# Kernel tuning notes

Hardware: AMD Instinct MI355X
Metric: run time of the kernel (lower is better)

## Reference

```python
import jax, jax.numpy as jnp
import numpy as np

N, S, W, H = 256, 64, 256, 32   # node_num, sensor_num, slide_win, gru_hid_size
ALPHA = 0.2
NEG = -9e15


def gat(h, adj, Wm, a):
    """pyGAT GraphAttentionLayer (concat=False, dropout=0 / eval).
    h: [..., M, din], adj: [..., M, M], Wm: [..., din, dout], a: [..., 2*dout]."""
    Wh = jnp.einsum('...mi,...io->...mo', h, Wm)
    dout = Wm.shape[-1]
    f1 = jnp.einsum('...mo,...o->...m', Wh, a[..., :dout])
    f2 = jnp.einsum('...mo,...o->...m', Wh, a[..., dout:])
    e = jax.nn.leaky_relu(f1[..., :, None] + f2[..., None, :], negative_slope=ALPHA)
    att = jax.nn.softmax(jnp.where(adj > 0, e, NEG), axis=-1)
    return jnp.einsum('...mk,...ko->...mo', att, Wh)


def gru_cell(h, x, Wih, Whh, bih, bhh):
    # per-node batched torch GRU cell; gate order r, z, n
    gi = jnp.einsum('ngi,ni->ng', Wih, x) + bih
    gh = jnp.einsum('ngh,nh->ng', Whh, h) + bhh
    ir, iz, inn = jnp.split(gi, 3, axis=-1)
    hr, hz, hn = jnp.split(gh, 3, axis=-1)
    r = jax.nn.sigmoid(ir + hr)
    z = jax.nn.sigmoid(iz + hz)
    n = jnp.tanh(inn + r * hn)
    return (1.0 - z) * n + z * h


def gru2(xseq, h0, Wih0, Whh0, bih0, bhh0, Wih1, Whh1, bih1, bhh1):
    # xseq: [N, S, Din] (seq axis = sensor axis), h0: [2, N, H] -> ([N,S,H], [2,N,H])
    def step(carry, x_t):
        h0c, h1c = carry
        h0n = gru_cell(h0c, x_t, Wih0, Whh0, bih0, bhh0)
        h1n = gru_cell(h1c, h0n, Wih1, Whh1, bih1, bhh1)
        return (h0n, h1n), h1n
    (h0f, h1f), ys = jax.lax.scan(step, (h0[0], h0[1]), jnp.swapaxes(xseq, 0, 1))
    return jnp.swapaxes(ys, 0, 1), jnp.stack([h0f, h1f])


def setup_inputs():
    key = jax.random.key(0)
    ks = jax.random.split(key, 32)
    def rn(k, shape, scale=0.05):
        return jax.random.normal(k, shape, dtype=jnp.float32) * scale
    inp = {}
    inp['x'] = jax.random.normal(ks[0], (N, S, W), dtype=jnp.float32)
    inp['Feature_adj_sub'] = jax.random.randint(ks[1], (N, S, S), 0, 2).astype(jnp.float32)
    inp['Time_adj_sub'] = jax.random.randint(ks[2], (N, W, W), 0, 2).astype(jnp.float32)
    inp['adj'] = jax.random.randint(ks[3], (N, N), 0, 2).astype(jnp.float32)
    inp['H_pre'] = jax.random.normal(ks[4], (2, N, H), dtype=jnp.float32)
    # per-node GAT params (stacked over nodes)
    inp['Fatt_W'] = rn(ks[5], (N, W, W)); inp['Fatt_a'] = rn(ks[6], (N, 2 * W))
    inp['Tatt_W'] = rn(ks[7], (N, S, S)); inp['Tatt_a'] = rn(ks[8], (N, 2 * S))
    # per-node 2-layer GRU params
    inp['Wih0'] = rn(ks[9], (N, 3 * H, 3 * W)); inp['Whh0'] = rn(ks[10], (N, 3 * H, H))
    inp['bih0'] = rn(ks[11], (N, 3 * H)); inp['bhh0'] = rn(ks[12], (N, 3 * H))
    inp['Wih1'] = rn(ks[13], (N, 3 * H, H)); inp['Whh1'] = rn(ks[14], (N, 3 * H, H))
    inp['bih1'] = rn(ks[15], (N, 3 * H)); inp['bhh1'] = rn(ks[16], (N, 3 * H))
    # per-node 3-layer FC
    inp['fc1_w'] = rn(ks[17], (N, H, H)); inp['fc1_b'] = rn(ks[18], (N, H))
    inp['fc2_w'] = rn(ks[19], (N, H, H)); inp['fc2_b'] = rn(ks[20], (N, H))
    inp['fc3_w'] = rn(ks[21], (N, 1, H)); inp['fc3_b'] = rn(ks[22], (N, 1))
    # global output GATs
    inp['oW'] = rn(ks[23], (S, S)); inp['oa'] = rn(ks[24], (2 * S,))
    inp['o1W'] = rn(ks[25], (S, S)); inp['o1a'] = rn(ks[26], (2 * S,))
    inp['o2W'] = rn(ks[27], (2 * S, S)); inp['o2a'] = rn(ks[28], (2 * S,))
    return inp


def reference(x, Feature_adj_sub, Time_adj_sub, adj, H_pre,
              Fatt_W, Fatt_a, Tatt_W, Tatt_a,
              Wih0, Whh0, bih0, bhh0, Wih1, Whh1, bih1, bhh1,
              fc1_w, fc1_b, fc2_w, fc2_b, fc3_w, fc3_b,
              oW, oa, o1W, o1a, o2W, o2a):
    # batched over all nodes at once (replaces Python loop over node_num)
    Fat = gat(x, Feature_adj_sub, Fatt_W, Fatt_a)                    # [N,S,W]
    Tat = gat(jnp.swapaxes(x, 1, 2), Time_adj_sub, Tatt_W, Tatt_a)   # [N,W,S]
    cat_at = jnp.concatenate([Fat, jnp.swapaxes(Tat, 1, 2), x], axis=-1)  # [N,S,3W]
    gru_out, cat_H = gru2(cat_at, H_pre, Wih0, Whh0, bih0, bhh0,
                          Wih1, Whh1, bih1, bhh1)                    # [N,S,H],[2,N,H]
    h = jax.nn.relu(jnp.einsum('nsh,nkh->nsk', gru_out, fc1_w) + fc1_b[:, None, :])
    h = jax.nn.relu(jnp.einsum('nsh,nkh->nsk', h, fc2_w) + fc2_b[:, None, :])
    ct = (jnp.einsum('nsh,nkh->nsk', h, fc3_w) + fc3_b[:, None, :])[..., 0]  # [N,S]
    out = gat(ct, adj, oW, oa)
    out1 = gat(ct, adj, o1W, o1a)
    finalout = gat(jnp.concatenate([out, out1], axis=-1), adj, o2W, o2a)
    return finalout, cat_H
```

## Files before the change

kernel.cpp:

```cpp
#include <hip/hip_runtime.h>
#include <hip/hip_bf16.h>

__device__ __forceinline__ float sigf(float x){ return __builtin_amdgcn_rcpf(1.f+__expf(-x)); }
__device__ __forceinline__ float tanhfa(float x){
  return 1.f - 2.f*__builtin_amdgcn_rcpf(1.f + __expf(2.f*x));
}

#define ALPHA 0.2f
#define NEGV  -9e15f


__device__ __forceinline__ void gl2lds16(const float* g, float* l){
  __builtin_amdgcn_global_load_lds(
      (const __attribute__((address_space(1))) void*)g,
      (__attribute__((address_space(3))) void*)l, 16, 0, 0);
}

__global__ __launch_bounds__(256) void k_mask(const float* __restrict__ src,
                                              unsigned* __restrict__ dst, int nelem){
  const int stride = gridDim.x * blockDim.x;
  const int lane = threadIdx.x & 63;
  for (int e = blockIdx.x*blockDim.x + threadIdx.x; e < nelem; e += stride){
    unsigned long long m = __ballot(src[e] > 0.f);
    if (lane == 0)       dst[e >> 5] = (unsigned)m;
    else if (lane == 32) dst[e >> 5] = (unsigned)(m >> 32);
  }
}

__global__ __launch_bounds__(256) void k3_wht(const float* __restrict__ x,
                                              const float* __restrict__ TW,
                                              const float* __restrict__ Ta,
                                              float* __restrict__ WhTt,
                                              float* __restrict__ Tf1p,
                                              float* __restrict__ Tf2p){
  const int n = blockIdx.x >> 1, ch = blockIdx.x & 1, c0 = ch*32;
  const int tid = threadIdx.x;
  __shared__ float Wm[64][36];
  __shared__ float as1[32], as2[32];
  for (int idx = tid; idx < 2048; idx += 256){
    int k = idx >> 5, cc = idx & 31;
    Wm[k][cc] = TW[n*4096 + k*64 + c0 + cc];
  }
  if (tid < 32){ as1[tid] = Ta[n*128 + c0 + tid]; as2[tid] = Ta[n*128 + 64 + c0 + tid]; }
  __syncthreads();
  const int i = tid;
  const float* xn = x + n*16384;
  float acc[32];
#pragma unroll
  for (int c = 0; c < 32; ++c) acc[c] = 0.f;
#pragma unroll 2
  for (int k = 0; k < 64; ++k){
    float xv = xn[k*256 + i];
    const float* wr = &Wm[k][0];
#pragma unroll
    for (int c = 0; c < 32; ++c) acc[c] = fmaf(xv, wr[c], acc[c]);
  }
  float f1 = 0.f, f2 = 0.f;
#pragma unroll
  for (int c = 0; c < 32; ++c){ f1 = fmaf(acc[c], as1[c], f1); f2 = fmaf(acc[c], as2[c], f2); }
  Tf1p[ch*65536 + n*256 + i] = f1;
  Tf2p[ch*65536 + n*256 + i] = f2;
  float* o = WhTt + n*16384;
#pragma unroll
  for (int c = 0; c < 32; ++c) o[(c0+c)*256 + i] = acc[c];
}

__global__ __launch_bounds__(256) void k4_tat(const float* __restrict__ WhTt,
                                              const float* __restrict__ Tf1p,
                                              const float* __restrict__ Tf2p,
                                              const unsigned* __restrict__ maskT,
                                              float* __restrict__ TatT){
  const int n = blockIdx.x >> 1, ch = blockIdx.x & 1, c0 = ch*32;
  const int i = threadIdx.x;
  __shared__ float wt[8192];
  __shared__ float f2s[256];
  __shared__ float wmax[4];
  {
    const int w = i >> 6, l = i & 63;
    const float* src = WhTt + n*16384 + c0*256 + w*2048 + l*4;
    float* dst = &wt[w*2048];
#pragma unroll
    for (int r = 0; r < 8; ++r) gl2lds16(src + r*256, dst + r*256);
  }
  const float f1  = Tf1p[n*256 + i] + Tf1p[65536 + n*256 + i];
  const float f2v = Tf2p[n*256 + i] + Tf2p[65536 + n*256 + i];
  f2s[i] = f2v;
  unsigned mw[8];
#pragma unroll
  for (int w = 0; w < 8; ++w) mw[w] = maskT[n*2048 + i*8 + w];
  float wm = f2v;
#pragma unroll
  for (int d = 1; d < 64; d <<= 1) wm = fmaxf(wm, __shfl_xor(wm, d));
  if ((i & 63) == 0) wmax[i >> 6] = wm;
  asm volatile("s_waitcnt vmcnt(0)" ::: "memory");
  __syncthreads();
  const float mb = fmaxf(fmaxf(wmax[0], wmax[1]), fmaxf(wmax[2], wmax[3]));
  const float tm = f1 + mb;
  const float m  = (tm > 0.f) ? tm : ALPHA*tm;
  float acc[32];
#pragma unroll
  for (int c = 0; c < 32; ++c) acc[c] = 0.f;
  float s = 0.f;
#pragma unroll 2
  for (int jb = 0; jb < 64; ++jb){
    const float4 f2q = *(const float4*)&f2s[jb*4];
    const unsigned mk = mw[jb >> 3];
    const int sh = (jb & 7) * 4;
    float t0 = f1 + f2q.x; t0 = (t0 > 0.f) ? t0 : ALPHA*t0;
    float t1 = f1 + f2q.y; t1 = (t1 > 0.f) ? t1 : ALPHA*t1;
    float t2 = f1 + f2q.z; t2 = (t2 > 0.f) ? t2 : ALPHA*t2;
    float t3 = f1 + f2q.w; t3 = (t3 > 0.f) ? t3 : ALPHA*t3;
    const float e0 = ((mk >> (sh+0)) & 1u) ? __expf(t0 - m) : 0.f;
    const float e1 = ((mk >> (sh+1)) & 1u) ? __expf(t1 - m) : 0.f;
    const float e2 = ((mk >> (sh+2)) & 1u) ? __expf(t2 - m) : 0.f;
    const float e3 = ((mk >> (sh+3)) & 1u) ? __expf(t3 - m) : 0.f;
    s += (e0 + e1) + (e2 + e3);
#pragma unroll
    for (int c = 0; c < 32; ++c){
      const float4 wv = *(const float4*)&wt[c*256 + jb*4];
      acc[c] = fmaf(e0, wv.x, fmaf(e1, wv.y, fmaf(e2, wv.z, fmaf(e3, wv.w, acc[c]))));
    }
  }
  const float inv = (s > 0.f) ? __builtin_amdgcn_rcpf(s) : 0.f;
  float* o = TatT + n*16384;
#pragma unroll
  for (int c = 0; c < 32; ++c) o[(c0+c)*256 + i] = acc[c] * inv;
}

__global__ __launch_bounds__(256) void k1_whf(const float* __restrict__ x,
                                              const float* __restrict__ FW,
                                              float* __restrict__ WhF){
  const int n = blockIdx.x >> 1, ch = blockIdx.x & 1, c0 = ch*128;
  const int tid = threadIdx.x;
  __shared__ float xt[16384];
  {
    const int w = tid >> 6, l = tid & 63;
    const float* xg = x + n*16384 + w*4096 + l*4;
    float* ld = &xt[w*4096];
#pragma unroll
    for (int j = 0; j < 16; ++j) gl2lds16(xg + j*256, ld + j*256);
  }
  asm volatile("s_waitcnt vmcnt(0)" ::: "memory");
  __syncthreads();
  const int cq = tid & 31, iq = tid >> 5;
  const int cc = c0 + cq*4;
  const float* Wn = FW + (size_t)n*65536 + cc;
  const float* xrow = &xt[iq*8*256];
  float acc[8][4];
#pragma unroll
  for (int i = 0; i < 8; ++i)
#pragma unroll
    for (int c = 0; c < 4; ++c) acc[i][c] = 0.f;
#pragma unroll 2
  for (int k4 = 0; k4 < 64; ++k4){
    const float4 w0 = *(const float4*)&Wn[(4*k4+0)*256];
    const float4 w1 = *(const float4*)&Wn[(4*k4+1)*256];
    const float4 w2 = *(const float4*)&Wn[(4*k4+2)*256];
    const float4 w3 = *(const float4*)&Wn[(4*k4+3)*256];
#pragma unroll
    for (int i = 0; i < 8; ++i){
      const float4 xv = *(const float4*)&xrow[i*256 + 4*k4];
      acc[i][0] = fmaf(xv.x, w0.x, acc[i][0]); acc[i][0] = fmaf(xv.y, w1.x, acc[i][0]);
      acc[i][0] = fmaf(xv.z, w2.x, acc[i][0]); acc[i][0] = fmaf(xv.w, w3.x, acc[i][0]);
      acc[i][1] = fmaf(xv.x, w0.y, acc[i][1]); acc[i][1] = fmaf(xv.y, w1.y, acc[i][1]);
      acc[i][1] = fmaf(xv.z, w2.y, acc[i][1]); acc[i][1] = fmaf(xv.w, w3.y, acc[i][1]);
      acc[i][2] = fmaf(xv.x, w0.z, acc[i][2]); acc[i][2] = fmaf(xv.y, w1.z, acc[i][2]);
      acc[i][2] = fmaf(xv.z, w2.z, acc[i][2]); acc[i][2] = fmaf(xv.w, w3.z, acc[i][2]);
      acc[i][3] = fmaf(xv.x, w0.w, acc[i][3]); acc[i][3] = fmaf(xv.y, w1.w, acc[i][3]);
      acc[i][3] = fmaf(xv.z, w2.w, acc[i][3]); acc[i][3] = fmaf(xv.w, w3.w, acc[i][3]);
    }
  }
  float* o = WhF + n*16384 + cc;
#pragma unroll
  for (int i = 0; i < 8; ++i)
    *(float4*)&o[(iq*8 + i)*256] = make_float4(acc[i][0], acc[i][1], acc[i][2], acc[i][3]);
}

__global__ __launch_bounds__(512) void k2_fat(const float* __restrict__ WhF,
                                              const float* __restrict__ Fa,
                                              const float* __restrict__ Fadj,
                                              float* __restrict__ Fat){
  const int n = blockIdx.x, tid = threadIdx.x;
  __shared__ float attT[64][68];
  __shared__ float f1s[64], f2s[64];
  __shared__ float part[64][8][2];
  const float* Wh = WhF + n*16384;
  {
    int i = tid >> 3, q = tid & 7;
    const float* an = Fa + n*512;
    float p1 = 0.f, p2 = 0.f;
    for (int cc = 0; cc < 32; ++cc){
      int c2 = q*32 + cc;
      float w = Wh[i*256 + c2];
      p1 = fmaf(w, an[c2], p1);
      p2 = fmaf(w, an[256 + c2], p2);
    }
    part[i][q][0] = p1; part[i][q][1] = p2;
  }
  __syncthreads();
  if (tid < 64){
    float s1 = 0.f, s2 = 0.f;
#pragma unroll
    for (int q = 0; q < 8; ++q){ s1 += part[tid][q][0]; s2 += part[tid][q][1]; }
    f1s[tid] = s1; f2s[tid] = s2;
  }
  __syncthreads();
  if (tid < 64){
    const int r = tid;
    const float f1 = f1s[r];
    const float* adjr = Fadj + n*4096 + r*64;
    unsigned m0 = 0, m1 = 0;
#pragma unroll
    for (int j = 0; j < 32; ++j) if (adjr[j] > 0.f) m0 |= (1u << j);
#pragma unroll
    for (int j = 0; j < 32; ++j) if (adjr[32+j] > 0.f) m1 |= (1u << j);
    float m = -INFINITY;
#pragma unroll
    for (int j = 0; j < 64; ++j){
      float e = f1 + f2s[j]; e = (e > 0.f) ? e : ALPHA*e;
      unsigned bit = (j < 32) ? ((m0 >> j) & 1u) : ((m1 >> (j-32)) & 1u);
      e = bit ? e : NEGV;
      m = fmaxf(m, e);
    }
    float s = 0.f;
#pragma unroll
    for (int j = 0; j < 64; ++j){
      float e = f1 + f2s[j]; e = (e > 0.f) ? e : ALPHA*e;
      unsigned bit = (j < 32) ? ((m0 >> j) & 1u) : ((m1 >> (j-32)) & 1u);
      e = bit ? e : NEGV;
      s += __expf(e - m);
    }
    const float inv = 1.f / s;
#pragma unroll
    for (int j = 0; j < 64; ++j){
      float e = f1 + f2s[j]; e = (e > 0.f) ? e : ALPHA*e;
      unsigned bit = (j < 32) ? ((m0 >> j) & 1u) : ((m1 >> (j-32)) & 1u);
      e = bit ? e : NEGV;
      attT[j][r] = __expf(e - m) * inv;
    }
  }
  __syncthreads();
  const int c = tid & 255, ih = tid >> 8;
  float acc[32];
#pragma unroll
  for (int i = 0; i < 32; ++i) acc[i] = 0.f;
#pragma unroll 2
  for (int j = 0; j < 64; ++j){
    float w = Wh[j*256 + c];
    const float* ar = &attT[j][ih*32];
#pragma unroll
    for (int i = 0; i < 32; ++i) acc[i] = fmaf(ar[i], w, acc[i]);
  }
  float* o = Fat + n*16384;
#pragma unroll
  for (int i = 0; i < 32; ++i) o[(ih*32 + i)*256 + c] = acc[i];
}

__global__ __launch_bounds__(256) void k5_gi0(const float* __restrict__ Fat,
                                              const float* __restrict__ TatT,
                                              const float* __restrict__ x,
                                              const float* __restrict__ Wih0,
                                              float* __restrict__ P0,
                                              float* __restrict__ P1,
                                              float* __restrict__ P2){
  const int n = blockIdx.x & 255, s = blockIdx.x >> 8;
  const int tid = threadIdx.x;
  const int l = tid & 63, w = tid >> 6;
  const int a = tid & 31, b = tid >> 5;
  __shared__ float cl[2][2048];
  __shared__ float wl[2][3072];
  const float* src = (s == 0) ? (Fat + n*16384)
                   : (s == 1) ? (TatT + n*16384)
                              : (x + n*16384);
  const float* Wseg = Wih0 + (size_t)n*73728 + s*256;
  const int lr = l >> 3, lc = l & 7, sc = lc ^ lr;
  const float* cg0 = src + (16*w + lr)*256 + sc*4;
  const float* cg1 = cg0 + 8*256;
  const float* wg0 = Wseg + (size_t)(24*w + lr)*768 + lc*4;
  const float* wg1 = wg0 + (size_t)8*768;
  const float* wg2 = wg0 + (size_t)16*768;

#define K5_STAGE(BF, K0) do {                       \
    gl2lds16(cg0 + (K0), &cl[BF][512*w]);           \
    gl2lds16(cg1 + (K0), &cl[BF][512*w + 256]);     \
    gl2lds16(wg0 + (K0), &wl[BF][768*w]);           \
    gl2lds16(wg1 + (K0), &wl[BF][768*w + 256]);     \
    gl2lds16(wg2 + (K0), &wl[BF][768*w + 512]);     \
  } while (0)

  float acc[12][2];
#pragma unroll
  for (int gi = 0; gi < 12; ++gi){ acc[gi][0] = 0.f; acc[gi][1] = 0.f; }

  int bf = 0;
  K5_STAGE(0, 0);
  const int ax4 = (a & 7) << 2;
#pragma unroll 1
  for (int kt = 0; kt < 8; ++kt){
    if (kt < 7){
      K5_STAGE(bf ^ 1, (kt + 1) * 32);
      asm volatile("s_waitcnt vmcnt(5)" ::: "memory");
    } else {
      asm volatile("s_waitcnt vmcnt(0)" ::: "memory");
    }
    __builtin_amdgcn_s_barrier();
    const float* clb  = &cl[bf][a*32];
    const float* clb2 = &cl[bf][(a+32)*32];
    const float* wlb  = &wl[bf][b*384];
#pragma unroll
    for (int k4 = 0; k4 < 8; ++k4){
      const int j4 = (k4 << 2) ^ ax4;
      const float4 c0 = *(const float4*)&clb[j4];
      const float4 c1 = *(const float4*)&clb2[j4];
#pragma unroll
      for (int gi = 0; gi < 12; ++gi){
        const float4 wv = *(const float4*)&wlb[gi*32 + (k4 << 2)];
        float a0 = acc[gi][0], a1 = acc[gi][1];
        a0 = fmaf(wv.x, c0.x, a0); a1 = fmaf(wv.x, c1.x, a1);
        a0 = fmaf(wv.y, c0.y, a0); a1 = fmaf(wv.y, c1.y, a1);
        a0 = fmaf(wv.z, c0.z, a0); a1 = fmaf(wv.z, c1.z, a1);
        a0 = fmaf(wv.w, c0.w, a0); a1 = fmaf(wv.w, c1.w, a1);
        acc[gi][0] = a0; acc[gi][1] = a1;
      }
    }
    __builtin_amdgcn_s_barrier();
    bf ^= 1;
  }
#undef K5_STAGE
  float* o = (s == 0) ? (P0 + n*16384)
           : (s == 1) ? (P1 + n*16384)
                      : (P2 + n*8192);
#pragma unroll
  for (int q = 0; q < 3; ++q){
    *(float4*)&o[a*96 + b*12 + q*4] =
        make_float4(acc[4*q][0], acc[4*q+1][0], acc[4*q+2][0], acc[4*q+3][0]);
    *(float4*)&o[(a+32)*96 + b*12 + q*4] =
        make_float4(acc[4*q][1], acc[4*q+1][1], acc[4*q+2][1], acc[4*q+3][1]);
  }
}

__global__ __launch_bounds__(128) void k6_gru(const float* __restrict__ G0,
                                              const float* __restrict__ G1,
                                              const float* __restrict__ G2,
                                              const float* __restrict__ Hpre,
                                              const float* __restrict__ Whh0,
                                              const float* __restrict__ bih0,
                                              const float* __restrict__ bhh0,
                                              const float* __restrict__ Wih1,
                                              const float* __restrict__ Whh1,
                                              const float* __restrict__ bih1,
                                              const float* __restrict__ bhh1,
                                              const float* __restrict__ fc1w,
                                              const float* __restrict__ fc1b,
                                              const float* __restrict__ fc2w,
                                              const float* __restrict__ fc2b,
                                              const float* __restrict__ fc3w,
                                              const float* __restrict__ fc3b,
                                              float* __restrict__ ct,
                                              float* __restrict__ dout){
  const int n = blockIdx.x, tid = threadIdx.x;
  const int wid = tid >> 6, l = tid & 63;
  const int g2 = l & 31, co = (l >> 5) * 16;
  __shared__ float ginS[6144];
  __shared__ float h0buf[2][32];
  __shared__ float h1buf[2][32];
  __shared__ float hist[64][33];
  __shared__ float Wst[32][33];
  __shared__ float b1s[32], b2s[32], w3s[32];
  {
    const float4* p0 = (const float4*)(G0 + n*16384);
    const float4* p1 = (const float4*)(G1 + n*16384);
    const float4* p2 = (const float4*)(G2 + n*8192);
    float4* gs = (float4*)ginS;
#pragma unroll
    for (int j = 0; j < 12; ++j){
      int idx = j*128 + tid;
      float4 a = p0[idx], b = p1[idx], c = p2[idx];
      gs[idx] = make_float4(a.x+b.x+c.x, a.y+b.y+c.y, a.z+b.z+c.z, a.w+b.w+c.w);
    }
  }
  if (tid < 32){
    b1s[tid] = fc1b[n*32 + tid];
    b2s[tid] = fc2b[n*32 + tid];
    w3s[tid] = fc3w[n*32 + tid];
  }
  for (int idx = tid; idx < 1024; idx += 128) Wst[idx>>5][idx&31] = fc1w[n*1024 + idx];
  float wr_[16], wz_[16], wn_[16];
  float ur_[16], uz_[16], un_[16];
  {
    const float* WA = (wid == 0) ? (Whh0 + n*3072) : (Wih1 + n*3072);
#pragma unroll
    for (int q = 0; q < 4; ++q){
      float4 v;
      v = *(const float4*)(WA + g2*32 + co + 4*q);       wr_[4*q]=v.x; wr_[4*q+1]=v.y; wr_[4*q+2]=v.z; wr_[4*q+3]=v.w;
      v = *(const float4*)(WA + (32+g2)*32 + co + 4*q);  wz_[4*q]=v.x; wz_[4*q+1]=v.y; wz_[4*q+2]=v.z; wz_[4*q+3]=v.w;
      v = *(const float4*)(WA + (64+g2)*32 + co + 4*q);  wn_[4*q]=v.x; wn_[4*q+1]=v.y; wn_[4*q+2]=v.z; wn_[4*q+3]=v.w;
    }
    if (wid == 1){
      const float* WB = Whh1 + n*3072;
#pragma unroll
      for (int q = 0; q < 4; ++q){
        float4 v;
        v = *(const float4*)(WB + g2*32 + co + 4*q);       ur_[4*q]=v.x; ur_[4*q+1]=v.y; ur_[4*q+2]=v.z; ur_[4*q+3]=v.w;
        v = *(const float4*)(WB + (32+g2)*32 + co + 4*q);  uz_[4*q]=v.x; uz_[4*q+1]=v.y; uz_[4*q+2]=v.z; uz_[4*q+3]=v.w;
        v = *(const float4*)(WB + (64+g2)*32 + co + 4*q);  un_[4*q]=v.x; un_[4*q+1]=v.y; un_[4*q+2]=v.z; un_[4*q+3]=v.w;
      }
    }
  }
  const float* bip = (wid == 0) ? bih0 : bih1;
  const float* bhp = (wid == 0) ? bhh0 : bhh1;
  const float br = bip[n*96 + g2], bz = bip[n*96 + 32 + g2], bn = bip[n*96 + 64 + g2];
  const float cr = bhp[n*96 + g2], cz = bhp[n*96 + 32 + g2], cn = bhp[n*96 + 64 + g2];
  const float* hp = (wid == 0) ? (Hpre + n*32) : (Hpre + 8192 + n*32);
  float hown = hp[g2];
  float hs[16];
#pragma unroll
  for (int q = 0; q < 4; ++q){
    float4 v = *(const float4*)&hp[co + 4*q];
    hs[4*q]=v.x; hs[4*q+1]=v.y; hs[4*q+2]=v.z; hs[4*q+3]=v.w;
  }
  for (int s = 0; s < 65; ++s){
    __syncthreads();
    if (wid == 0){
      if (s < 64){
        const float gr = ginS[s*96 + g2], gz = ginS[s*96 + 32 + g2], gn = ginS[s*96 + 64 + g2];
        if (s > 0){
#pragma unroll
          for (int q = 0; q < 4; ++q){
            float4 v = *(const float4*)&h0buf[(s-1)&1][co + 4*q];
            hs[4*q]=v.x; hs[4*q+1]=v.y; hs[4*q+2]=v.z; hs[4*q+3]=v.w;
          }
        }
        float pr = 0.f, pz = 0.f, pn = 0.f;
#pragma unroll
        for (int j = 0; j < 16; ++j){
          pr = fmaf(wr_[j], hs[j], pr);
          pz = fmaf(wz_[j], hs[j], pz);
          pn = fmaf(wn_[j], hs[j], pn);
        }
        pr += __shfl_xor(pr, 32);
        pz += __shfl_xor(pz, 32);
        pn += __shfl_xor(pn, 32);
        const float r = sigf(gr + br + pr + cr);
        const float z = sigf(gz + bz + pz + cz);
        const float nn = tanhfa(gn + bn + r*(pn + cn));
        hown = (1.f - z)*nn + z*hown;
        if (l < 32) h0buf[s & 1][g2] = hown;
      }
    } else {
      if (s >= 1){
        const int t = s - 1;
        if (s > 1){
#pragma unroll
          for (int q = 0; q < 4; ++q){
            float4 v = *(const float4*)&h1buf[(s-1)&1][co + 4*q];
            hs[4*q]=v.x; hs[4*q+1]=v.y; hs[4*q+2]=v.z; hs[4*q+3]=v.w;
          }
        }
        float hx[16];
#pragma unroll
        for (int q = 0; q < 4; ++q){
          float4 v = *(const float4*)&h0buf[(s-1)&1][co + 4*q];
          hx[4*q]=v.x; hx[4*q+1]=v.y; hx[4*q+2]=v.z; hx[4*q+3]=v.w;
        }
        float qr = 0.f, qz = 0.f, qn = 0.f, sr = 0.f, sz = 0.f, sn = 0.f;
#pragma unroll
        for (int j = 0; j < 16; ++j){
          qr = fmaf(wr_[j], hx[j], qr);  sr = fmaf(ur_[j], hs[j], sr);
          qz = fmaf(wz_[j], hx[j], qz);  sz = fmaf(uz_[j], hs[j], sz);
          qn = fmaf(wn_[j], hx[j], qn);  sn = fmaf(un_[j], hs[j], sn);
        }
        float vr = qr + sr; vr += __shfl_xor(vr, 32);
        float vz = qz + sz; vz += __shfl_xor(vz, 32);
        qn += __shfl_xor(qn, 32);
        sn += __shfl_xor(sn, 32);
        const float r1 = sigf(vr + br + cr);
        const float z1 = sigf(vz + bz + cz);
        const float n1 = tanhfa(qn + bn + r1*(sn + cn));
        hown = (1.f - z1)*n1 + z1*hown;
        if (l < 32){ h1buf[s & 1][g2] = hown; hist[t][g2] = hown; }
      }
    }
  }
  if (wid == 0 && l < 32) dout[16384 + n*32 + g2] = hown;
  if (wid == 1 && l < 32) dout[16384 + 8192 + n*32 + g2] = hown;
  __syncthreads();
  float r1a[32];
  if (tid < 64){
    float hr[32];
#pragma unroll
    for (int k = 0; k < 32; ++k) hr[k] = hist[tid][k];
#pragma unroll
    for (int k = 0; k < 32; ++k){
      float a0=0.f,a1=0.f,a2=0.f,a3=0.f;
#pragma unroll
      for (int q = 0; q < 32; q += 4){
        a0 = fmaf(hr[q],   Wst[k][q],   a0);
        a1 = fmaf(hr[q+1], Wst[k][q+1], a1);
        a2 = fmaf(hr[q+2], Wst[k][q+2], a2);
        a3 = fmaf(hr[q+3], Wst[k][q+3], a3);
      }
      float v = b1s[k] + ((a0+a1)+(a2+a3));
      r1a[k] = v > 0.f ? v : 0.f;
    }
  }
  __syncthreads();
  for (int idx = tid; idx < 1024; idx += 128) Wst[idx>>5][idx&31] = fc2w[n*1024 + idx];
  __syncthreads();
  if (tid < 64){
    float r2a[32];
#pragma unroll
    for (int k = 0; k < 32; ++k){
      float a0=0.f,a1=0.f,a2=0.f,a3=0.f;
#pragma unroll
      for (int q = 0; q < 32; q += 4){
        a0 = fmaf(r1a[q],   Wst[k][q],   a0);
        a1 = fmaf(r1a[q+1], Wst[k][q+1], a1);
        a2 = fmaf(r1a[q+2], Wst[k][q+2], a2);
        a3 = fmaf(r1a[q+3], Wst[k][q+3], a3);
      }
      float v = b2s[k] + ((a0+a1)+(a2+a3));
      r2a[k] = v > 0.f ? v : 0.f;
    }
    float v = fc3b[n];
#pragma unroll
    for (int k = 0; k < 32; ++k) v = fmaf(r2a[k], w3s[k], v);
    ct[n*64 + tid] = v;
  }
}

__global__ __launch_bounds__(256) void k8a(const float* __restrict__ ct,
                                           const float* __restrict__ W0,
                                           const float* __restrict__ a0,
                                           const float* __restrict__ W1,
                                           const float* __restrict__ a1,
                                           float* __restrict__ WhABt,
                                           float* __restrict__ OF1,
                                           float* __restrict__ OF2){
  const int gat = blockIdx.x >> 2, rq = blockIdx.x & 3, r0 = rq*64;
  const int tid = threadIdx.x;
  const int ii = tid & 63, cq = tid >> 6;
  __shared__ float ctl[64][65];
  __shared__ float Wl[64][68];
  __shared__ float a1s[64], a2s[64];
  __shared__ float red[64][4][2];
  const float* W = gat ? W1 : W0;
  const float* aa = gat ? a1 : a0;
  for (int idx = tid; idx < 4096; idx += 256){
    int i2 = idx >> 6, k = idx & 63;
    ctl[i2][k] = ct[(r0 + i2)*64 + k];
  }
  for (int idx = tid; idx < 4096; idx += 256){
    int k = idx >> 6, c = idx & 63;
    Wl[k][c] = W[k*64 + c];
  }
  if (tid < 64){ a1s[tid] = aa[tid]; a2s[tid] = aa[64 + tid]; }
  __syncthreads();
  float acc[16];
#pragma unroll
  for (int c = 0; c < 16; ++c) acc[c] = 0.f;
#pragma unroll 2
  for (int k = 0; k < 64; ++k){
    float v = ctl[ii][k];
    const float* wr = &Wl[k][cq*16];
#pragma unroll
    for (int c = 0; c < 16; ++c) acc[c] = fmaf(v, wr[c], acc[c]);
  }
  float p1 = 0.f, p2 = 0.f;
#pragma unroll
  for (int c = 0; c < 16; ++c){
    p1 = fmaf(acc[c], a1s[cq*16 + c], p1);
    p2 = fmaf(acc[c], a2s[cq*16 + c], p2);
  }
  red[ii][cq][0] = p1; red[ii][cq][1] = p2;
  float* o = WhABt + gat*16384;
#pragma unroll
  for (int c = 0; c < 16; ++c) o[(cq*16 + c)*256 + r0 + ii] = acc[c];
  __syncthreads();
  if (cq == 0){
    OF1[gat*256 + r0 + ii] = red[ii][0][0] + red[ii][1][0] + red[ii][2][0] + red[ii][3][0];
    OF2[gat*256 + r0 + ii] = red[ii][0][1] + red[ii][1][1] + red[ii][2][1] + red[ii][3][1];
  }
}

__global__ __launch_bounds__(256) void k8b(const float* __restrict__ WhABt,
                                           const float* __restrict__ OF1,
                                           const float* __restrict__ OF2,
                                           const unsigned* __restrict__ maskA,
                                           float* __restrict__ OUTT){
  const int gat = blockIdx.x >> 2, c0 = (blockIdx.x & 3) * 16;
  const int i = threadIdx.x;
  __shared__ float wt[4096];
  __shared__ float f2s[256];
  __shared__ float wmax[4];
  {
    const int w = i >> 6, l = i & 63;
    const float* src = WhABt + gat*16384 + c0*256 + w*1024 + l*4;
    float* dst = &wt[w*1024];
#pragma unroll
    for (int r = 0; r < 4; ++r) gl2lds16(src + r*256, dst + r*256);
  }
  const float f1  = OF1[gat*256 + i];
  const float f2v = OF2[gat*256 + i];
  f2s[i] = f2v;
  unsigned mw[8];
#pragma unroll
  for (int w = 0; w < 8; ++w) mw[w] = maskA[i*8 + w];
  float wm = f2v;
#pragma unroll
  for (int d = 1; d < 64; d <<= 1) wm = fmaxf(wm, __shfl_xor(wm, d));
  if ((i & 63) == 0) wmax[i >> 6] = wm;
  asm volatile("s_waitcnt vmcnt(0)" ::: "memory");
  __syncthreads();
  const float mb = fmaxf(fmaxf(wmax[0], wmax[1]), fmaxf(wmax[2], wmax[3]));
  const float tm = f1 + mb;
  const float m  = (tm > 0.f) ? tm : ALPHA*tm;
  float acc[16];
#pragma unroll
  for (int c = 0; c < 16; ++c) acc[c] = 0.f;
  float s = 0.f;
#pragma unroll 2
  for (int jb = 0; jb < 64; ++jb){
    const float4 f2q = *(const float4*)&f2s[jb*4];
    const unsigned mk = mw[jb >> 3];
    const int sh = (jb & 7) * 4;
    float t0 = f1 + f2q.x; t0 = (t0 > 0.f) ? t0 : ALPHA*t0;
    float t1 = f1 + f2q.y; t1 = (t1 > 0.f) ? t1 : ALPHA*t1;
    float t2 = f1 + f2q.z; t2 = (t2 > 0.f) ? t2 : ALPHA*t2;
    float t3 = f1 + f2q.w; t3 = (t3 > 0.f) ? t3 : ALPHA*t3;
    const float e0 = ((mk >> (sh+0)) & 1u) ? __expf(t0 - m) : 0.f;
    const float e1 = ((mk >> (sh+1)) & 1u) ? __expf(t1 - m) : 0.f;
    const float e2 = ((mk >> (sh+2)) & 1u) ? __expf(t2 - m) : 0.f;
    const float e3 = ((mk >> (sh+3)) & 1u) ? __expf(t3 - m) : 0.f;
    s += (e0 + e1) + (e2 + e3);
#pragma unroll
    for (int c = 0; c < 16; ++c){
      const float4 wv = *(const float4*)&wt[c*256 + jb*4];
      acc[c] = fmaf(e0, wv.x, fmaf(e1, wv.y, fmaf(e2, wv.z, fmaf(e3, wv.w, acc[c]))));
    }
  }
  const float inv = (s > 0.f) ? __builtin_amdgcn_rcpf(s) : 0.f;
#pragma unroll
  for (int c = 0; c < 16; ++c) OUTT[gat*16384 + (c0+c)*256 + i] = acc[c] * inv;
}

__global__ __launch_bounds__(256) void k8c(const float* __restrict__ OUTT,
                                           const float* __restrict__ W2,
                                           const float* __restrict__ a2,
                                           float* __restrict__ Wh2,
                                           float* __restrict__ F1B,
                                           float* __restrict__ F2B){
  const int r0 = blockIdx.x * 32;
  const int tid = threadIdx.x;
  const int ii = tid & 31, cq = tid >> 5;
  __shared__ float W2l[128][68];
  __shared__ float a1s[64], a2s[64];
  __shared__ float red[32][8][2];
  for (int idx = tid; idx < 8192; idx += 256){
    int k = idx >> 6, c = idx & 63;
    W2l[k][c] = W2[k*64 + c];
  }
  if (tid < 64){ a1s[tid] = a2[tid]; a2s[tid] = a2[64 + tid]; }
  __syncthreads();
  float acc[8];
#pragma unroll
  for (int c = 0; c < 8; ++c) acc[c] = 0.f;
#pragma unroll 2
  for (int k = 0; k < 128; ++k){
    float v = OUTT[(k >> 6)*16384 + (k & 63)*256 + r0 + ii];
    const float* wr = &W2l[k][cq*8];
#pragma unroll
    for (int c = 0; c < 8; ++c) acc[c] = fmaf(v, wr[c], acc[c]);
  }
  float p1 = 0.f, p2 = 0.f;
#pragma unroll
  for (int c = 0; c < 8; ++c){
    p1 = fmaf(acc[c], a1s[cq*8 + c], p1);
    p2 = fmaf(acc[c], a2s[cq*8 + c], p2);
  }
  red[ii][cq][0] = p1; red[ii][cq][1] = p2;
#pragma unroll
  for (int c = 0; c < 8; ++c) Wh2[(cq*8 + c)*256 + r0 + ii] = acc[c];
  __syncthreads();
  if (cq == 0){
    float s1 = 0.f, s2 = 0.f;
#pragma unroll
    for (int q = 0; q < 8; ++q){ s1 += red[ii][q][0]; s2 += red[ii][q][1]; }
    F1B[r0 + ii] = s1; F2B[r0 + ii] = s2;
  }
}

__global__ __launch_bounds__(256) void k8d(const float* __restrict__ Wh2,
                                           const float* __restrict__ F1B,
                                           const float* __restrict__ F2B,
                                           const unsigned* __restrict__ maskA,
                                           float* __restrict__ dOut){
  const int c0 = blockIdx.x * 16;
  const int i = threadIdx.x;
  __shared__ float wt[4096];
  __shared__ float f2s[256];
  __shared__ float wmax[4];
  {
    const int w = i >> 6, l = i & 63;
    const float* src = Wh2 + c0*256 + w*1024 + l*4;
    float* dst = &wt[w*1024];
#pragma unroll
    for (int r = 0; r < 4; ++r) gl2lds16(src + r*256, dst + r*256);
  }
  const float f1  = F1B[i];
  const float f2v = F2B[i];
  f2s[i] = f2v;
  unsigned mw[8];
#pragma unroll
  for (int w = 0; w < 8; ++w) mw[w] = maskA[i*8 + w];
  float wm = f2v;
#pragma unroll
  for (int d = 1; d < 64; d <<= 1) wm = fmaxf(wm, __shfl_xor(wm, d));
  if ((i & 63) == 0) wmax[i >> 6] = wm;
  asm volatile("s_waitcnt vmcnt(0)" ::: "memory");
  __syncthreads();
  const float mb = fmaxf(fmaxf(wmax[0], wmax[1]), fmaxf(wmax[2], wmax[3]));
  const float tm = f1 + mb;
  const float m  = (tm > 0.f) ? tm : ALPHA*tm;
  float acc[16];
#pragma unroll
  for (int c = 0; c < 16; ++c) acc[c] = 0.f;
  float s = 0.f;
#pragma unroll 2
  for (int jb = 0; jb < 64; ++jb){
    const float4 f2q = *(const float4*)&f2s[jb*4];
    const unsigned mk = mw[jb >> 3];
    const int sh = (jb & 7) * 4;
    float t0 = f1 + f2q.x; t0 = (t0 > 0.f) ? t0 : ALPHA*t0;
    float t1 = f1 + f2q.y; t1 = (t1 > 0.f) ? t1 : ALPHA*t1;
    float t2 = f1 + f2q.z; t2 = (t2 > 0.f) ? t2 : ALPHA*t2;
    float t3 = f1 + f2q.w; t3 = (t3 > 0.f) ? t3 : ALPHA*t3;
    const float e0 = ((mk >> (sh+0)) & 1u) ? __expf(t0 - m) : 0.f;
    const float e1 = ((mk >> (sh+1)) & 1u) ? __expf(t1 - m) : 0.f;
    const float e2 = ((mk >> (sh+2)) & 1u) ? __expf(t2 - m) : 0.f;
    const float e3 = ((mk >> (sh+3)) & 1u) ? __expf(t3 - m) : 0.f;
    s += (e0 + e1) + (e2 + e3);
#pragma unroll
    for (int c = 0; c < 16; ++c){
      const float4 wv = *(const float4*)&wt[c*256 + jb*4];
      acc[c] = fmaf(e0, wv.x, fmaf(e1, wv.y, fmaf(e2, wv.z, fmaf(e3, wv.w, acc[c]))));
    }
  }
  const float inv = (s > 0.f) ? __builtin_amdgcn_rcpf(s) : 0.f;
#pragma unroll
  for (int c = 0; c < 16; ++c) dOut[i*64 + c0 + c] = acc[c] * inv;
}

extern "C" void kernel_launch(void* const* d_in, const int* in_sizes, int n_in,
                              void* d_out, int out_size, void* d_ws, size_t ws_size,
                              hipStream_t stream){
  (void)in_sizes; (void)n_in; (void)out_size; (void)ws_size;
  const float* x     = (const float*)d_in[0];
  const float* Fadj  = (const float*)d_in[1];
  const float* Tadj  = (const float*)d_in[2];
  const float* adj   = (const float*)d_in[3];
  const float* Hpre  = (const float*)d_in[4];
  const float* FattW = (const float*)d_in[5];
  const float* Fatta = (const float*)d_in[6];
  const float* TattW = (const float*)d_in[7];
  const float* Tatta = (const float*)d_in[8];
  const float* Wih0  = (const float*)d_in[9];
  const float* Whh0  = (const float*)d_in[10];
  const float* bih0  = (const float*)d_in[11];
  const float* bhh0  = (const float*)d_in[12];
  const float* Wih1  = (const float*)d_in[13];
  const float* Whh1  = (const float*)d_in[14];
  const float* bih1  = (const float*)d_in[15];
  const float* bhh1  = (const float*)d_in[16];
  const float* fc1w  = (const float*)d_in[17];
  const float* fc1b  = (const float*)d_in[18];
  const float* fc2w  = (const float*)d_in[19];
  const float* fc2b  = (const float*)d_in[20];
  const float* fc3w  = (const float*)d_in[21];
  const float* fc3b  = (const float*)d_in[22];
  const float* oW    = (const float*)d_in[23];
  const float* oa    = (const float*)d_in[24];
  const float* o1W   = (const float*)d_in[25];
  const float* o1a   = (const float*)d_in[26];
  const float* o2W   = (const float*)d_in[27];
  const float* o2a   = (const float*)d_in[28];
  float* out = (float*)d_out;

  float* ws = (float*)d_ws;
  float* R0 = ws;
  float* R1 = ws + 4194304;
  float* R2 = ws + 8388608;
  unsigned* maskT = (unsigned*)R2;
  float* Tf1p = R2 + 524288;
  float* Tf2p = R2 + 655360;
  unsigned* maskA = (unsigned*)(ws + 12582912);
  float* WhTt = R0;
  float* WhF  = R0;
  float* TatT = R1;
  float* Fat  = R2;
  float* P0 = R2;
  float* P1 = R1;
  float* P2 = R0;
  float* ctb   = R0 + 2097152;
  float* WhABt = R1 + 16384;
  float* OF1   = R1 + 49152;
  float* OF2   = R1 + 49664;
  float* OUTT  = R1 + 50176;
  float* WH2   = R1 + 82944;
  float* F1B   = R1 + 99328;
  float* F2B   = R1 + 99584;

  k_mask<<<1024, 256, 0, stream>>>(Tadj, maskT, 16777216);
  k_mask<<<32, 256, 0, stream>>>(adj, maskA, 65536);
  k3_wht<<<512, 256, 0, stream>>>(x, TattW, Tatta, WhTt, Tf1p, Tf2p);
  k4_tat<<<512, 256, 0, stream>>>(WhTt, Tf1p, Tf2p, maskT, TatT);
  k1_whf<<<512, 256, 0, stream>>>(x, FattW, WhF);
  k2_fat<<<256, 512, 0, stream>>>(WhF, Fatta, Fadj, Fat);
  k5_gi0<<<768, 256, 0, stream>>>(Fat, TatT, x, Wih0, P0, P1, P2);
  k6_gru<<<256, 128, 0, stream>>>(P0, P1, P2, Hpre, Whh0, bih0, bhh0, Wih1, Whh1, bih1, bhh1,
                                  fc1w, fc1b, fc2w, fc2b, fc3w, fc3b, ctb, out);
  k8a<<<8, 256, 0, stream>>>(ctb, oW, oa, o1W, o1a, WhABt, OF1, OF2);
  k8b<<<8, 256, 0, stream>>>(WhABt, OF1, OF2, maskA, OUTT);
  k8c<<<8, 256, 0, stream>>>(OUTT, o2W, o2a, WH2, F1B, F2B);
  k8d<<<4, 256, 0, stream>>>(WH2, F1B, F2B, maskA, out);
}
```

Before: 631.4 us.

## Retile time-attention aggregation as register-blocked 4x8 outer product via LDS

The WhT intermediate is now stored node-major (row i holds its 64 channels), written as float4 vectors. The Tat kernel first computes the masked softmax numerators into an LDS tile of 32 keys at a time. It then does the attention-times-Wh product as a 4-row by 8-channel register-blocked outer product per thread. This raises FMA-to-LDS-load reuse compared with the old per-row scheme, where every thread read 32 float4s per key group. It costs an extra 32KB of LDS, more barriers, and scattered output stores.

Result: faster. 605.2 us (-4.2%).

```diff
diff --git a/kernel.cpp b/kernel.cpp
--- a/kernel.cpp
+++ b/kernel.cpp
@@ -60,9 +60,10 @@
   for (int c = 0; c < 32; ++c){ f1 = fmaf(acc[c], as1[c], f1); f2 = fmaf(acc[c], as2[c], f2); }
   Tf1p[ch*65536 + n*256 + i] = f1;
   Tf2p[ch*65536 + n*256 + i] = f2;
-  float* o = WhTt + n*16384;
-#pragma unroll
-  for (int c = 0; c < 32; ++c) o[(c0+c)*256 + i] = acc[c];
+  float* o = WhTt + n*16384 + i*64 + c0;
+#pragma unroll
+  for (int q = 0; q < 8; ++q)
+    *(float4*)&o[4*q] = make_float4(acc[4*q], acc[4*q+1], acc[4*q+2], acc[4*q+3]);
 }
 
 __global__ __launch_bounds__(256) void k4_tat(const float* __restrict__ WhTt,
@@ -71,60 +72,95 @@
                                               const unsigned* __restrict__ maskT,
                                               float* __restrict__ TatT){
   const int n = blockIdx.x >> 1, ch = blockIdx.x & 1, c0 = ch*32;
-  const int i = threadIdx.x;
-  __shared__ float wt[8192];
+  const int tid = threadIdx.x;
+  __shared__ float wtL[8192];
+  __shared__ float ptb[8192];
   __shared__ float f2s[256];
+  __shared__ float ssum[256];
   __shared__ float wmax[4];
   {
-    const int w = i >> 6, l = i & 63;
-    const float* src = WhTt + n*16384 + c0*256 + w*2048 + l*4;
-    float* dst = &wt[w*2048];
-#pragma unroll
-    for (int r = 0; r < 8; ++r) gl2lds16(src + r*256, dst + r*256);
-  }
-  const float f1  = Tf1p[n*256 + i] + Tf1p[65536 + n*256 + i];
-  const float f2v = Tf2p[n*256 + i] + Tf2p[65536 + n*256 + i];
-  f2s[i] = f2v;
+    const int w = tid >> 6, l = tid & 63;
+    const float* src = WhTt + n*16384 + (w*64 + (l>>3))*64 + c0 + (l&7)*4;
+    float* dst = &wtL[w*2048];
+#pragma unroll
+    for (int r = 0; r < 8; ++r) gl2lds16(src + r*512, dst + r*256);
+  }
+  const float f1  = Tf1p[n*256 + tid] + Tf1p[65536 + n*256 + tid];
+  const float f2v = Tf2p[n*256 + tid] + Tf2p[65536 + n*256 + tid];
+  f2s[tid] = f2v;
   unsigned mw[8];
 #pragma unroll
-  for (int w = 0; w < 8; ++w) mw[w] = maskT[n*2048 + i*8 + w];
+  for (int w = 0; w < 8; ++w) mw[w] = maskT[n*2048 + tid*8 + w];
   float wm = f2v;
 #pragma unroll
   for (int d = 1; d < 64; d <<= 1) wm = fmaxf(wm, __shfl_xor(wm, d));
-  if ((i & 63) == 0) wmax[i >> 6] = wm;
+  if ((tid & 63) == 0) wmax[tid >> 6] = wm;
   asm volatile("s_waitcnt vmcnt(0)" ::: "memory");
   __syncthreads();
   const float mb = fmaxf(fmaxf(wmax[0], wmax[1]), fmaxf(wmax[2], wmax[3]));
   const float tm = f1 + mb;
   const float m  = (tm > 0.f) ? tm : ALPHA*tm;
-  float acc[32];
-#pragma unroll
-  for (int c = 0; c < 32; ++c) acc[c] = 0.f;
-  float s = 0.f;
-#pragma unroll 2
-  for (int jb = 0; jb < 64; ++jb){
-    const float4 f2q = *(const float4*)&f2s[jb*4];
-    const unsigned mk = mw[jb >> 3];
-    const int sh = (jb & 7) * 4;
-    float t0 = f1 + f2q.x; t0 = (t0 > 0.f) ? t0 : ALPHA*t0;
-    float t1 = f1 + f2q.y; t1 = (t1 > 0.f) ? t1 : ALPHA*t1;
-    float t2 = f1 + f2q.z; t2 = (t2 > 0.f) ? t2 : ALPHA*t2;
-    float t3 = f1 + f2q.w; t3 = (t3 > 0.f) ? t3 : ALPHA*t3;
-    const float e0 = ((mk >> (sh+0)) & 1u) ? __expf(t0 - m) : 0.f;
-    const float e1 = ((mk >> (sh+1)) & 1u) ? __expf(t1 - m) : 0.f;
-    const float e2 = ((mk >> (sh+2)) & 1u) ? __expf(t2 - m) : 0.f;
-    const float e3 = ((mk >> (sh+3)) & 1u) ? __expf(t3 - m) : 0.f;
-    s += (e0 + e1) + (e2 + e3);
-#pragma unroll
-    for (int c = 0; c < 32; ++c){
-      const float4 wv = *(const float4*)&wt[c*256 + jb*4];
-      acc[c] = fmaf(e0, wv.x, fmaf(e1, wv.y, fmaf(e2, wv.z, fmaf(e3, wv.w, acc[c]))));
-    }
-  }
-  const float inv = (s > 0.f) ? __builtin_amdgcn_rcpf(s) : 0.f;
+  const int iq = tid & 63, cq = tid >> 6;
+  float acc[4][8];
+#pragma unroll
+  for (int r = 0; r < 4; ++r)
+#pragma unroll
+    for (int c = 0; c < 8; ++c) acc[r][c] = 0.f;
+  float sloc = 0.f;
+  for (int jt = 0; jt < 8; ++jt){
+    const int j0 = jt*32;
+#pragma unroll
+    for (int jj = 0; jj < 32; jj += 4){
+      const float4 f2q = *(const float4*)&f2s[j0 + jj];
+      const unsigned mk = mw[(j0 + jj) >> 5];
+      const int sh = (j0 + jj) & 31;
+      float t0 = f1 + f2q.x; t0 = (t0 > 0.f) ? t0 : ALPHA*t0;
+      float t1 = f1 + f2q.y; t1 = (t1 > 0.f) ? t1 : ALPHA*t1;
+      float t2 = f1 + f2q.z; t2 = (t2 > 0.f) ? t2 : ALPHA*t2;
+      float t3 = f1 + f2q.w; t3 = (t3 > 0.f) ? t3 : ALPHA*t3;
+      const float e0 = ((mk >> (sh+0)) & 1u) ? __expf(t0 - m) : 0.f;
+      const float e1 = ((mk >> (sh+1)) & 1u) ? __expf(t1 - m) : 0.f;
+      const float e2 = ((mk >> (sh+2)) & 1u) ? __expf(t2 - m) : 0.f;
+      const float e3 = ((mk >> (sh+3)) & 1u) ? __expf(t3 - m) : 0.f;
+      sloc += (e0 + e1) + (e2 + e3);
+      ptb[(jj+0)*256 + tid] = e0;
+      ptb[(jj+1)*256 + tid] = e1;
+      ptb[(jj+2)*256 + tid] = e2;
+      ptb[(jj+3)*256 + tid] = e3;
+    }
+    __syncthreads();
+#pragma unroll 4
+    for (int jj = 0; jj < 32; ++jj){
+      const float4 p4 = *(const float4*)&ptb[jj*256 + 4*iq];
+      const float4 w0 = *(const float4*)&wtL[(j0+jj)*32 + cq*8];
+      const float4 w1 = *(const float4*)&wtL[(j0+jj)*32 + cq*8 + 4];
+#pragma unroll
+      for (int r = 0; r < 4; ++r){
+        const float pv = (r == 0) ? p4.x : (r == 1) ? p4.y : (r == 2) ? p4.z : p4.w;
+        acc[r][0] = fmaf(pv, w0.x, acc[r][0]);
+        acc[r][1] = fmaf(pv, w0.y, acc[r][1]);
+        acc[r][2] = fmaf(pv, w0.z, acc[r][2]);
+        acc[r][3] = fmaf(pv, w0.w, acc[r][3]);
+        acc[r][4] = fmaf(pv, w1.x, acc[r][4]);
+        acc[r][5] = fmaf(pv, w1.y, acc[r][5]);
+        acc[r][6] = fmaf(pv, w1.z, acc[r][6]);
+        acc[r][7] = fmaf(pv, w1.w, acc[r][7]);
+      }
+    }
+    __syncthreads();
+  }
+  ssum[tid] = sloc;
+  __syncthreads();
   float* o = TatT + n*16384;
 #pragma unroll
-  for (int c = 0; c < 32; ++c) o[(c0+c)*256 + i] = acc[c] * inv;
+  for (int r = 0; r < 4; ++r){
+    const int i2 = 4*iq + r;
+    const float sv = ssum[i2];
+    const float inv = (sv > 0.f) ? __builtin_amdgcn_rcpf(sv) : 0.f;
+#pragma unroll
+    for (int cc = 0; cc < 8; ++cc)
+      o[(c0 + cq*8 + cc)*256 + i2] = acc[r][cc] * inv;
+  }
 }
 
 __global__ __launch_bounds__(256) void k1_whf(const float* __restrict__ x,
```
